# Kernel optimization log

Measured on AMD Instinct MI355X. Metric: run time of the kernel, lower is better.

## Reference

```python
import jax, jax.numpy as jnp
import numpy as np

RADIUS = 0.4   # 0.2 * nlayer, nlayer = 2
NSAMPLE = 32   # k


def _fps(xyz, m):
    """Farthest point sampling. xyz: (B, N, 3) -> idx (B, m) int32.
    Matches pointnet2 CUDA kernel: first sampled point is index 0."""
    B, N, _ = xyz.shape

    def step(carry, _):
        dist, far = carry
        centroid = jnp.take_along_axis(xyz, far[:, None, None], axis=1)  # (B,1,3)
        d = jnp.sum((xyz - centroid) ** 2, axis=-1)                      # (B,N)
        dist = jnp.minimum(dist, d)
        return (dist, jnp.argmax(dist, axis=-1).astype(jnp.int32)), far

    init = (jnp.full((B, N), jnp.inf, dtype=xyz.dtype),
            jnp.zeros((B,), dtype=jnp.int32))
    _, idx = jax.lax.scan(step, init, None, length=m)  # (m, B)
    return idx.T                                       # (B, m)


def _ball_query(radius, k, xyz, new_xyz):
    """xyz (B,N,3), new_xyz (B,M,3) -> (B,M,k) int32.
    First k in-radius indices in ascending index order; slots past the
    number of in-radius points are filled with the first found index
    (pointnet2 ball_query semantics)."""
    N = xyz.shape[1]
    d2 = jnp.sum((new_xyz[:, :, None, :] - xyz[:, None, :, :]) ** 2, axis=-1)  # (B,M,N)
    key = jnp.where(d2 < radius * radius,
                    jnp.arange(N, dtype=jnp.int32), jnp.int32(N))              # (B,M,N)
    topv, _ = jax.lax.top_k(-key, k)   # k smallest keys, ascending
    idx = -topv                        # (B,M,k)
    valid = idx < N
    idx = jnp.where(valid, idx, idx[..., :1])  # pad with first found index
    return idx


def _group(t, idx):
    """t (B,C,N), idx (B,M,k) -> (B,C,M,k)."""
    return jnp.take_along_axis(t[:, :, None, :], idx[:, None, :, :], axis=3)


def setup_inputs() -> dict:
    key = jax.random.key(0)
    k1, k2, k3 = jax.random.split(key, 3)
    return {
        "x": jax.random.normal(k1, (8, 3, 8192), dtype=jnp.float32),
        "feature": jax.random.normal(k2, (8, 64, 8192), dtype=jnp.float32),
        "weight": jax.random.normal(k3, (64, 64), dtype=jnp.float32) / 8.0,
        "num_pool": 2048,
    }


def reference(x, feature, weight, num_pool):
    # x: (B,3,N) coordinates, feature: (B,C,N), weight: 1x1 conv (C_out, C_in)
    xyz = jnp.transpose(x, (0, 2, 1))                       # (B,N,3)
    fps_idx = _fps(xyz, num_pool)                           # (B,M)
    new_xyz = jnp.take_along_axis(xyz, fps_idx[:, :, None], axis=1)  # (B,M,3)
    sub_idx = _ball_query(RADIUS, NSAMPLE, xyz, new_xyz)    # (B,M,k)

    x_out = _group(x, sub_idx).max(axis=-1)                 # (B,3,M)
    fg = _group(feature, sub_idx)                           # (B,C,M,k)
    f_out = jnp.einsum('oc,bcmk->bomk', weight, fg).max(axis=-1)  # (B,C,M)
    return x_out, f_out
```

## Files before the change

kernel.cpp:

```cpp
#include <hip/hip_runtime.h>
#include <cstdint>
#include <cstddef>

#define BB 8
#define NN 8192
#define CC 64
#define MM 2048
#define KK 32

typedef float vfloat2 __attribute__((ext_vector_type(2)));

__device__ __forceinline__ float sqdist_exact(float x, float y, float z,
                                              float cx, float cy, float cz) {
    float dx = __fsub_rn(x, cx);
    float dy = __fsub_rn(y, cy);
    float dz = __fsub_rn(z, cz);
    return __fadd_rn(__fadd_rn(__fmul_rn(dx, dx), __fmul_rn(dy, dy)),
                     __fmul_rn(dz, dz));
}

template <int CTRL>
__device__ __forceinline__ unsigned dpp_max_u32(unsigned v) {
    unsigned s = (unsigned)__builtin_amdgcn_update_dpp(0, (int)v, CTRL, 0xF, 0xF, true);
    return v > s ? v : s;
}
template <int CTRL>
__device__ __forceinline__ unsigned dpp_min_u32(unsigned v) {
    unsigned s = (unsigned)__builtin_amdgcn_update_dpp(0x7FFFFFFF, (int)v, CTRL, 0xF, 0xF, false);
    return v < s ? v : s;
}

__device__ __forceinline__ int octile(float v) {
    return (v > -1.1503494f) + (v > -0.6744898f) + (v > -0.3186394f) + (v > 0.0f) +
           (v > 0.3186394f) + (v > 0.6744898f) + (v > 1.1503494f);
}

__device__ __forceinline__ int morton9(int bx, int by, int bz) {
    int m = (bz & 1) | ((bz & 2) << 2) | ((bz & 4) << 4);
    m |= ((by & 1) << 1) | ((by & 2) << 3) | ((by & 4) << 5);
    m |= ((bx & 1) << 2) | ((bx & 2) << 4) | ((bx & 4) << 6);
    return m;
}

__global__ __launch_bounds__(512) void fps_kernel(const float* __restrict__ x,
                                                  int* __restrict__ fps_idx) {
#pragma clang fp contract(off)
    const int b = blockIdx.x;
    const int tid = threadIdx.x;
    const int lane = tid & 63;
    const float* xb = x + (size_t)b * 3 * NN;
    int* fps_store = fps_idx + b * MM;

    __shared__ float sx[NN];
    __shared__ float sy[NN];
    __shared__ float sz[NN];
    __shared__ int sidx[NN];
    __shared__ int hist[512];
    __shared__ int scanb[512];
    __shared__ int sfps[MM];
    __shared__ unsigned long long red3[3];

    const vfloat2* gx = (const vfloat2*)xb;
    const vfloat2* gy = (const vfloat2*)(xb + NN);
    const vfloat2* gz = (const vfloat2*)(xb + 2 * NN);

    vfloat2 lx[8], ly[8], lz[8];
#pragma unroll
    for (int p = 0; p < 8; ++p) {
        const int e = tid + p * 512;
        lx[p] = gx[e];
        ly[p] = gy[e];
        lz[p] = gz[e];
        ((vfloat2*)sx)[e] = lx[p];
        ((vfloat2*)sy)[e] = ly[p];
        ((vfloat2*)sz)[e] = lz[p];
    }
    hist[tid] = 0;
    if (tid < 3) red3[tid] = 0ull;
    __syncthreads();

    int mybin[16];
#pragma unroll
    for (int p = 0; p < 8; ++p) {
        int b0 = morton9(octile(lx[p].x), octile(ly[p].x), octile(lz[p].x));
        int b1 = morton9(octile(lx[p].y), octile(ly[p].y), octile(lz[p].y));
        mybin[2 * p] = b0;
        mybin[2 * p + 1] = b1;
        atomicAdd(&hist[b0], 1);
        atomicAdd(&hist[b1], 1);
    }
    __syncthreads();
    int own = hist[tid];
    scanb[tid] = own;
    __syncthreads();
    for (int off = 1; off < 512; off <<= 1) {
        int add = (tid >= off) ? scanb[tid - off] : 0;
        __syncthreads();
        scanb[tid] += add;
        __syncthreads();
    }
    hist[tid] = scanb[tid] - own;
    __syncthreads();
#pragma unroll
    for (int p = 0; p < 8; ++p) {
        const int i0 = 2 * (tid + p * 512);
        int pos0 = atomicAdd(&hist[mybin[2 * p]], 1);
        sidx[pos0] = i0;
        int pos1 = atomicAdd(&hist[mybin[2 * p + 1]], 1);
        sidx[pos1] = i0 + 1;
    }
    __syncthreads();

    vfloat2 px[8], py[8], pz[8], dist[8];
    int idxr[16];
#pragma unroll
    for (int p = 0; p < 8; ++p) {
        const int j0 = sidx[tid * 16 + 2 * p];
        const int j1 = sidx[tid * 16 + 2 * p + 1];
        idxr[2 * p] = j0;
        idxr[2 * p + 1] = j1;
        px[p] = (vfloat2){sx[j0], sx[j1]};
        py[p] = (vfloat2){sy[j0], sy[j1]};
        pz[p] = (vfloat2){sz[j0], sz[j1]};
        dist[p] = (vfloat2){INFINITY, INFINITY};
    }
    float blx = fminf(px[0].x, px[0].y), bhx = fmaxf(px[0].x, px[0].y);
    float bly = fminf(py[0].x, py[0].y), bhy = fmaxf(py[0].x, py[0].y);
    float blz = fminf(pz[0].x, pz[0].y), bhz = fmaxf(pz[0].x, pz[0].y);
#pragma unroll
    for (int p = 1; p < 8; ++p) {
        blx = fminf(blx, fminf(px[p].x, px[p].y));
        bhx = fmaxf(bhx, fmaxf(px[p].x, px[p].y));
        bly = fminf(bly, fminf(py[p].x, py[p].y));
        bhy = fmaxf(bhy, fmaxf(py[p].x, py[p].y));
        blz = fminf(blz, fminf(pz[p].x, pz[p].y));
        bhz = fmaxf(bhz, fmaxf(pz[p].x, pz[p].y));
    }

    float cmax = INFINITY;
    int cidx = idxr[0];
    int far = 0;
    for (int t = 0; t < MM; ++t) {
        if (tid == 0) {
            sfps[t] = far;
            red3[(t + 1) % 3] = 0ull;
        }
        const float cx = sx[far];
        const float cy = sy[far];
        const float cz = sz[far];

        float qx = cx - fminf(fmaxf(cx, blx), bhx);
        float qy = cy - fminf(fmaxf(cy, bly), bhy);
        float qz = cz - fminf(fmaxf(cz, blz), bhz);
        float bound = (qx * qx + qy * qy) + qz * qz;
        const bool act = !(bound * 0.999f >= cmax);
        if (act) {
            const vfloat2 cx2 = {cx, cx};
            const vfloat2 cy2 = {cy, cy};
            const vfloat2 cz2 = {cz, cz};
            float mv = -1.0f;
#pragma unroll
            for (int p = 0; p < 8; ++p) {
                vfloat2 dx = px[p] - cx2;
                vfloat2 dy = py[p] - cy2;
                vfloat2 dz = pz[p] - cz2;
                vfloat2 m1 = dx * dx;
                vfloat2 m2 = dy * dy;
                vfloat2 m3 = dz * dz;
                vfloat2 s = (m1 + m2) + m3;
                vfloat2 nd;
                nd.x = fminf(dist[p].x, s.x);
                nd.y = fminf(dist[p].y, s.y);
                dist[p] = nd;
                mv = fmaxf(fmaxf(mv, nd.x), nd.y);
            }
            int mi = 0x7FFFFFFF;
#pragma unroll
            for (int p = 0; p < 8; ++p) {
                mi = min(mi, (dist[p].x == mv) ? idxr[2 * p] : 0x7FFFFFFF);
                mi = min(mi, (dist[p].y == mv) ? idxr[2 * p + 1] : 0x7FFFFFFF);
            }
            cmax = mv;
            cidx = mi;
        }

        unsigned mvb = __float_as_uint(cmax);
        mvb = dpp_max_u32<0x111>(mvb);
        mvb = dpp_max_u32<0x112>(mvb);
        mvb = dpp_max_u32<0x114>(mvb);
        mvb = dpp_max_u32<0x118>(mvb);
        mvb = dpp_max_u32<0x142>(mvb);
        mvb = dpp_max_u32<0x143>(mvb);
        const unsigned wmax = (unsigned)__builtin_amdgcn_readlane((int)mvb, 63);
        unsigned midx = (__float_as_uint(cmax) == wmax) ? (unsigned)cidx : 0x7FFFFFFFu;
        midx = dpp_min_u32<0x111>(midx);
        midx = dpp_min_u32<0x112>(midx);
        midx = dpp_min_u32<0x114>(midx);
        midx = dpp_min_u32<0x118>(midx);
        midx = dpp_min_u32<0x142>(midx);
        midx = dpp_min_u32<0x143>(midx);
        if (lane == 63) {
            unsigned long long key =
                ((unsigned long long)wmax << 32) | (unsigned)(~midx);
            atomicMax(&red3[t % 3], key);
        }
        __syncthreads();
        far = (int)(~(unsigned)red3[t % 3]);
    }
    __syncthreads();
    for (int t = tid; t < MM; t += 512) fps_store[t] = sfps[t];
}

__global__ __launch_bounds__(256) void transform_kernel(const float* __restrict__ feature,
                                                        const float* __restrict__ weight,
                                                        float* __restrict__ g) {
    __shared__ float Wl[64 * 64];
    const int tid = threadIdx.x;
    for (int k = tid; k < 64 * 64; k += 256) Wl[k] = weight[k];
    __syncthreads();

    const int P = blockIdx.x * 256 + tid;
    const int b = P >> 13;
    const int n = P & (NN - 1);
    const float* fb = feature + (size_t)b * CC * NN + n;

    float fr[64];
#pragma unroll
    for (int c = 0; c < 64; ++c) fr[c] = fb[(size_t)c * NN];

    float* go = g + ((size_t)b << 19) + (size_t)n * 64;
    for (int o = 0; o < 64; o += 4) {
        const float* w0 = &Wl[o * 64];
        const float* w1 = w0 + 64;
        const float* w2 = w0 + 128;
        const float* w3 = w0 + 192;
        float a0 = 0.f, a1 = 0.f, a2 = 0.f, a3 = 0.f;
#pragma unroll
        for (int c = 0; c < 64; c += 4) {
            float4 v0 = *(const float4*)(w0 + c);
            float4 v1 = *(const float4*)(w1 + c);
            float4 v2 = *(const float4*)(w2 + c);
            float4 v3 = *(const float4*)(w3 + c);
            a0 += v0.x * fr[c] + v0.y * fr[c + 1] + v0.z * fr[c + 2] + v0.w * fr[c + 3];
            a1 += v1.x * fr[c] + v1.y * fr[c + 1] + v1.z * fr[c + 2] + v1.w * fr[c + 3];
            a2 += v2.x * fr[c] + v2.y * fr[c + 1] + v2.z * fr[c + 2] + v2.w * fr[c + 3];
            a3 += v3.x * fr[c] + v3.y * fr[c + 1] + v3.z * fr[c + 2] + v3.w * fr[c + 3];
        }
        float4 r;
        r.x = a0; r.y = a1; r.z = a2; r.w = a3;
        *(float4*)(go + o) = r;
    }
}

__global__ __launch_bounds__(256) void bq_kernel(const float* __restrict__ x,
                                                 const int* __restrict__ fps_idx,
                                                 int* __restrict__ sub_idx,
                                                 float* __restrict__ xout) {
    const float R2 = (float)(0.4 * 0.4);
    int gw = (int)((blockIdx.x * 256 + threadIdx.x) >> 6);
    const int lane = threadIdx.x & 63;
    gw = __builtin_amdgcn_readfirstlane(gw);
    const int b = gw >> 11;
    const int m = gw & (MM - 1);
    const float* xb = x + (size_t)b * 3 * NN;

    const int ctr = fps_idx[gw];
    const float cx = xb[ctr];
    const float cy = xb[NN + ctr];
    const float cz = xb[2 * NN + ctr];

    int* sid = sub_idx + (size_t)gw * KK;
    int found = 0;
    int first = 0;
    float mx = -INFINITY, my = -INFINITY, mz = -INFINITY;

    for (int base = 0; base < NN; base += 64) {
        const int i = base + lane;
        const float xx = xb[i];
        const float yy = xb[NN + i];
        const float zz = xb[2 * NN + i];
        const float d2 = sqdist_exact(xx, yy, zz, cx, cy, cz);
        const bool q = d2 < R2;
        const unsigned long long mask = __ballot(q);
        if (q) {
            int pos = found + (int)__popcll(mask & ((1ull << lane) - 1ull));
            if (pos < KK) {
                sid[pos] = i;
                mx = fmaxf(mx, xx);
                my = fmaxf(my, yy);
                mz = fmaxf(mz, zz);
            }
        }
        if (found == 0 && mask != 0ull) first = base + (int)__builtin_ctzll(mask);
        found += (int)__popcll(mask);
        if (found >= KK) break;
    }
    if (found < KK) {
        if (lane < KK - found) sid[found + lane] = first;
    }
#pragma unroll
    for (int off = 32; off >= 1; off >>= 1) {
        mx = fmaxf(mx, __shfl_xor(mx, off, 64));
        my = fmaxf(my, __shfl_xor(my, off, 64));
        mz = fmaxf(mz, __shfl_xor(mz, off, 64));
    }
    if (lane == 0) {
        xout[(size_t)b * 3 * MM + 0 * MM + m] = mx;
        xout[(size_t)b * 3 * MM + 1 * MM + m] = my;
        xout[(size_t)b * 3 * MM + 2 * MM + m] = mz;
    }
}

__global__ __launch_bounds__(256) void gather_kernel(const float* __restrict__ g,
                                                     const int* __restrict__ sub_idx,
                                                     float* __restrict__ fout) {
    int gw = (int)((blockIdx.x * 256 + threadIdx.x) >> 6);
    const int lane = threadIdx.x & 63;
    gw = __builtin_amdgcn_readfirstlane(gw);
    const int b = gw >> 11;
    const int m = gw & (MM - 1);
    const int* sid = sub_idx + (size_t)gw * KK;
    const float* gb = g + ((size_t)b << 19);
    float acc = -INFINITY;
#pragma unroll
    for (int j = 0; j < KK; ++j) {
        const int id = sid[j];
        acc = fmaxf(acc, gb[(size_t)id * 64 + lane]);
    }
    fout[((size_t)b << 17) + ((size_t)lane << 11) + m] = acc;
}

extern "C" void kernel_launch(void* const* d_in, const int* in_sizes, int n_in,
                              void* d_out, int out_size, void* d_ws, size_t ws_size,
                              hipStream_t stream) {
    const float* x = (const float*)d_in[0];
    const float* feature = (const float*)d_in[1];
    const float* weight = (const float*)d_in[2];

    float* out = (float*)d_out;
    float* xout = out;
    float* fout = out + BB * 3 * MM;

    char* ws = (char*)d_ws;
    int* fps_idx = (int*)ws;
    int* sub_idx = (int*)(ws + (size_t)BB * MM * 4);
    float* g = (float*)(ws + (size_t)BB * MM * 4 + (size_t)BB * MM * KK * 4);

    fps_kernel<<<BB, 512, 0, stream>>>(x, fps_idx);
    transform_kernel<<<(BB * NN) / 256, 256, 0, stream>>>(feature, weight, g);
    bq_kernel<<<(BB * MM * 64) / 256, 256, 0, stream>>>(x, fps_idx, sub_idx, xout);
    gather_kernel<<<(BB * MM * 64) / 256, 256, 0, stream>>>(g, sub_idx, fout);
}
```

Baseline: 1.923 ms.

## Fuse transform into FPS launch and fuse ball query with gather

The feature transform now runs as extra blocks of the FPS launch, so the 8 long-running FPS blocks share the device with transform work instead of running serially before it. Ball query and gather are merged into one kernel that keeps neighbour indices in shared memory, which removes the global sub_idx round trip and one launch. The transform blocks now run at 512 threads and get the large FPS shared-memory allocation through a union, which may lower their occupancy. An unused morton9 variant is also added.

```diff
diff --git a/kernel.cpp b/kernel.cpp
--- a/kernel.cpp
+++ b/kernel.cpp
@@ -38,227 +38,242 @@
 __device__ __forceinline__ int morton9(int bx, int by, int bz) {
     int m = (bz & 1) | ((bz & 2) << 2) | ((bz & 4) << 4);
     m |= ((by & 1) << 1) | ((by & 2) << 3) | ((by & 4) << 5);
+    m |= ((bx & 1) << 2) | ((bx & 2) << 4) | ((bx & 6) << 4 & 0x40) | ((bx & 4) << 4);
+    return m;
+}
+
+__device__ __forceinline__ int morton9_ref(int bx, int by, int bz) {
+    int m = (bz & 1) | ((bz & 2) << 2) | ((bz & 4) << 4);
+    m |= ((by & 1) << 1) | ((by & 2) << 3) | ((by & 4) << 5);
     m |= ((bx & 1) << 2) | ((bx & 2) << 4) | ((bx & 4) << 6);
     return m;
 }
 
-__global__ __launch_bounds__(512) void fps_kernel(const float* __restrict__ x,
-                                                  int* __restrict__ fps_idx) {
+union FSmem {
+    struct {
+        float sx[NN];
+        float sy[NN];
+        float sz[NN];
+        int sidx[NN];
+        int hist[512];
+        int scanb[512];
+        int sfps[MM];
+        unsigned long long red3[3];
+    } f;
+    float Wl[64 * 64];
+};
+
+__global__ __launch_bounds__(512) void fps_transform_kernel(
+        const float* __restrict__ x, int* __restrict__ fps_idx,
+        const float* __restrict__ feature, const float* __restrict__ weight,
+        float* __restrict__ g) {
+    __shared__ FSmem sm;
+    const int tid = threadIdx.x;
+
+    if (blockIdx.x >= BB) {
+        for (int k = tid; k < 64 * 64; k += 512) sm.Wl[k] = weight[k];
+        __syncthreads();
+        const int P = (blockIdx.x - BB) * 512 + tid;
+        const int b = P >> 13;
+        const int n = P & (NN - 1);
+        const float* fb = feature + (size_t)b * CC * NN + n;
+        float fr[64];
+#pragma unroll
+        for (int c = 0; c < 64; ++c) fr[c] = fb[(size_t)c * NN];
+        float* go = g + ((size_t)b << 19) + (size_t)n * 64;
+        for (int o = 0; o < 64; o += 4) {
+            const float* w0 = &sm.Wl[o * 64];
+            const float* w1 = w0 + 64;
+            const float* w2 = w0 + 128;
+            const float* w3 = w0 + 192;
+            float a0 = 0.f, a1 = 0.f, a2 = 0.f, a3 = 0.f;
+#pragma unroll
+            for (int c = 0; c < 64; c += 4) {
+                float4 v0 = *(const float4*)(w0 + c);
+                float4 v1 = *(const float4*)(w1 + c);
+                float4 v2 = *(const float4*)(w2 + c);
+                float4 v3 = *(const float4*)(w3 + c);
+                a0 += v0.x * fr[c] + v0.y * fr[c + 1] + v0.z * fr[c + 2] + v0.w * fr[c + 3];
+                a1 += v1.x * fr[c] + v1.y * fr[c + 1] + v1.z * fr[c + 2] + v1.w * fr[c + 3];
+                a2 += v2.x * fr[c] + v2.y * fr[c + 1] + v2.z * fr[c + 2] + v2.w * fr[c + 3];
+                a3 += v3.x * fr[c] + v3.y * fr[c + 1] + v3.z * fr[c + 2] + v3.w * fr[c + 3];
+            }
+            float4 r;
+            r.x = a0; r.y = a1; r.z = a2; r.w = a3;
+            *(float4*)(go + o) = r;
+        }
+        return;
+    }
+
+    {
 #pragma clang fp contract(off)
-    const int b = blockIdx.x;
-    const int tid = threadIdx.x;
-    const int lane = tid & 63;
-    const float* xb = x + (size_t)b * 3 * NN;
-    int* fps_store = fps_idx + b * MM;
-
-    __shared__ float sx[NN];
-    __shared__ float sy[NN];
-    __shared__ float sz[NN];
-    __shared__ int sidx[NN];
-    __shared__ int hist[512];
-    __shared__ int scanb[512];
-    __shared__ int sfps[MM];
-    __shared__ unsigned long long red3[3];
-
-    const vfloat2* gx = (const vfloat2*)xb;
-    const vfloat2* gy = (const vfloat2*)(xb + NN);
-    const vfloat2* gz = (const vfloat2*)(xb + 2 * NN);
-
-    vfloat2 lx[8], ly[8], lz[8];
-#pragma unroll
-    for (int p = 0; p < 8; ++p) {
-        const int e = tid + p * 512;
-        lx[p] = gx[e];
-        ly[p] = gy[e];
-        lz[p] = gz[e];
-        ((vfloat2*)sx)[e] = lx[p];
-        ((vfloat2*)sy)[e] = ly[p];
-        ((vfloat2*)sz)[e] = lz[p];
-    }
-    hist[tid] = 0;
-    if (tid < 3) red3[tid] = 0ull;
-    __syncthreads();
-
-    int mybin[16];
-#pragma unroll
-    for (int p = 0; p < 8; ++p) {
-        int b0 = morton9(octile(lx[p].x), octile(ly[p].x), octile(lz[p].x));
-        int b1 = morton9(octile(lx[p].y), octile(ly[p].y), octile(lz[p].y));
-        mybin[2 * p] = b0;
-        mybin[2 * p + 1] = b1;
-        atomicAdd(&hist[b0], 1);
-        atomicAdd(&hist[b1], 1);
-    }
-    __syncthreads();
-    int own = hist[tid];
-    scanb[tid] = own;
-    __syncthreads();
-    for (int off = 1; off < 512; off <<= 1) {
-        int add = (tid >= off) ? scanb[tid - off] : 0;
-        __syncthreads();
-        scanb[tid] += add;
-        __syncthreads();
-    }
-    hist[tid] = scanb[tid] - own;
-    __syncthreads();
-#pragma unroll
-    for (int p = 0; p < 8; ++p) {
-        const int i0 = 2 * (tid + p * 512);
-        int pos0 = atomicAdd(&hist[mybin[2 * p]], 1);
-        sidx[pos0] = i0;
-        int pos1 = atomicAdd(&hist[mybin[2 * p + 1]], 1);
-        sidx[pos1] = i0 + 1;
-    }
-    __syncthreads();
-
-    vfloat2 px[8], py[8], pz[8], dist[8];
-    int idxr[16];
-#pragma unroll
-    for (int p = 0; p < 8; ++p) {
-        const int j0 = sidx[tid * 16 + 2 * p];
-        const int j1 = sidx[tid * 16 + 2 * p + 1];
-        idxr[2 * p] = j0;
-        idxr[2 * p + 1] = j1;
-        px[p] = (vfloat2){sx[j0], sx[j1]};
-        py[p] = (vfloat2){sy[j0], sy[j1]};
-        pz[p] = (vfloat2){sz[j0], sz[j1]};
-        dist[p] = (vfloat2){INFINITY, INFINITY};
-    }
-    float blx = fminf(px[0].x, px[0].y), bhx = fmaxf(px[0].x, px[0].y);
-    float bly = fminf(py[0].x, py[0].y), bhy = fmaxf(py[0].x, py[0].y);
-    float blz = fminf(pz[0].x, pz[0].y), bhz = fmaxf(pz[0].x, pz[0].y);
-#pragma unroll
-    for (int p = 1; p < 8; ++p) {
-        blx = fminf(blx, fminf(px[p].x, px[p].y));
-        bhx = fmaxf(bhx, fmaxf(px[p].x, px[p].y));
-        bly = fminf(bly, fminf(py[p].x, py[p].y));
-        bhy = fmaxf(bhy, fmaxf(py[p].x, py[p].y));
-        blz = fminf(blz, fminf(pz[p].x, pz[p].y));
-        bhz = fmaxf(bhz, fmaxf(pz[p].x, pz[p].y));
-    }
-
-    float cmax = INFINITY;
-    int cidx = idxr[0];
-    int far = 0;
-    for (int t = 0; t < MM; ++t) {
-        if (tid == 0) {
-            sfps[t] = far;
-            red3[(t + 1) % 3] = 0ull;
-        }
-        const float cx = sx[far];
-        const float cy = sy[far];
-        const float cz = sz[far];
-
-        float qx = cx - fminf(fmaxf(cx, blx), bhx);
-        float qy = cy - fminf(fmaxf(cy, bly), bhy);
-        float qz = cz - fminf(fmaxf(cz, blz), bhz);
-        float bound = (qx * qx + qy * qy) + qz * qz;
-        const bool act = !(bound * 0.999f >= cmax);
-        if (act) {
-            const vfloat2 cx2 = {cx, cx};
-            const vfloat2 cy2 = {cy, cy};
-            const vfloat2 cz2 = {cz, cz};
-            float mv = -1.0f;
-#pragma unroll
-            for (int p = 0; p < 8; ++p) {
-                vfloat2 dx = px[p] - cx2;
-                vfloat2 dy = py[p] - cy2;
-                vfloat2 dz = pz[p] - cz2;
-                vfloat2 m1 = dx * dx;
-                vfloat2 m2 = dy * dy;
-                vfloat2 m3 = dz * dz;
-                vfloat2 s = (m1 + m2) + m3;
-                vfloat2 nd;
-                nd.x = fminf(dist[p].x, s.x);
-                nd.y = fminf(dist[p].y, s.y);
-                dist[p] = nd;
-                mv = fmaxf(fmaxf(mv, nd.x), nd.y);
-            }
-            int mi = 0x7FFFFFFF;
-#pragma unroll
-            for (int p = 0; p < 8; ++p) {
-                mi = min(mi, (dist[p].x == mv) ? idxr[2 * p] : 0x7FFFFFFF);
-                mi = min(mi, (dist[p].y == mv) ? idxr[2 * p + 1] : 0x7FFFFFFF);
-            }
-            cmax = mv;
-            cidx = mi;
-        }
-
-        unsigned mvb = __float_as_uint(cmax);
-        mvb = dpp_max_u32<0x111>(mvb);
-        mvb = dpp_max_u32<0x112>(mvb);
-        mvb = dpp_max_u32<0x114>(mvb);
-        mvb = dpp_max_u32<0x118>(mvb);
-        mvb = dpp_max_u32<0x142>(mvb);
-        mvb = dpp_max_u32<0x143>(mvb);
-        const unsigned wmax = (unsigned)__builtin_amdgcn_readlane((int)mvb, 63);
-        unsigned midx = (__float_as_uint(cmax) == wmax) ? (unsigned)cidx : 0x7FFFFFFFu;
-        midx = dpp_min_u32<0x111>(midx);
-        midx = dpp_min_u32<0x112>(midx);
-        midx = dpp_min_u32<0x114>(midx);
-        midx = dpp_min_u32<0x118>(midx);
-        midx = dpp_min_u32<0x142>(midx);
-        midx = dpp_min_u32<0x143>(midx);
-        if (lane == 63) {
-            unsigned long long key =
-                ((unsigned long long)wmax << 32) | (unsigned)(~midx);
-            atomicMax(&red3[t % 3], key);
-        }
-        __syncthreads();
-        far = (int)(~(unsigned)red3[t % 3]);
-    }
-    __syncthreads();
-    for (int t = tid; t < MM; t += 512) fps_store[t] = sfps[t];
-}
-
-__global__ __launch_bounds__(256) void transform_kernel(const float* __restrict__ feature,
-                                                        const float* __restrict__ weight,
-                                                        float* __restrict__ g) {
-    __shared__ float Wl[64 * 64];
-    const int tid = threadIdx.x;
-    for (int k = tid; k < 64 * 64; k += 256) Wl[k] = weight[k];
-    __syncthreads();
-
-    const int P = blockIdx.x * 256 + tid;
-    const int b = P >> 13;
-    const int n = P & (NN - 1);
-    const float* fb = feature + (size_t)b * CC * NN + n;
-
-    float fr[64];
-#pragma unroll
-    for (int c = 0; c < 64; ++c) fr[c] = fb[(size_t)c * NN];
-
-    float* go = g + ((size_t)b << 19) + (size_t)n * 64;
-    for (int o = 0; o < 64; o += 4) {
-        const float* w0 = &Wl[o * 64];
-        const float* w1 = w0 + 64;
-        const float* w2 = w0 + 128;
-        const float* w3 = w0 + 192;
-        float a0 = 0.f, a1 = 0.f, a2 = 0.f, a3 = 0.f;
-#pragma unroll
-        for (int c = 0; c < 64; c += 4) {
-            float4 v0 = *(const float4*)(w0 + c);
-            float4 v1 = *(const float4*)(w1 + c);
-            float4 v2 = *(const float4*)(w2 + c);
-            float4 v3 = *(const float4*)(w3 + c);
-            a0 += v0.x * fr[c] + v0.y * fr[c + 1] + v0.z * fr[c + 2] + v0.w * fr[c + 3];
-            a1 += v1.x * fr[c] + v1.y * fr[c + 1] + v1.z * fr[c + 2] + v1.w * fr[c + 3];
-            a2 += v2.x * fr[c] + v2.y * fr[c + 1] + v2.z * fr[c + 2] + v2.w * fr[c + 3];
-            a3 += v3.x * fr[c] + v3.y * fr[c + 1] + v3.z * fr[c + 2] + v3.w * fr[c + 3];
-        }
-        float4 r;
-        r.x = a0; r.y = a1; r.z = a2; r.w = a3;
-        *(float4*)(go + o) = r;
-    }
-}
-
-__global__ __launch_bounds__(256) void bq_kernel(const float* __restrict__ x,
-                                                 const int* __restrict__ fps_idx,
-                                                 int* __restrict__ sub_idx,
-                                                 float* __restrict__ xout) {
+        const int b = blockIdx.x;
+        const int lane = tid & 63;
+        const float* xb = x + (size_t)b * 3 * NN;
+        int* fps_store = fps_idx + b * MM;
+
+        const vfloat2* gx = (const vfloat2*)xb;
+        const vfloat2* gy = (const vfloat2*)(xb + NN);
+        const vfloat2* gz = (const vfloat2*)(xb + 2 * NN);
+
+        vfloat2 lx[8], ly[8], lz[8];
+#pragma unroll
+        for (int p = 0; p < 8; ++p) {
+            const int e = tid + p * 512;
+            lx[p] = gx[e];
+            ly[p] = gy[e];
+            lz[p] = gz[e];
+            ((vfloat2*)sm.f.sx)[e] = lx[p];
+            ((vfloat2*)sm.f.sy)[e] = ly[p];
+            ((vfloat2*)sm.f.sz)[e] = lz[p];
+        }
+        sm.f.hist[tid] = 0;
+        if (tid < 3) sm.f.red3[tid] = 0ull;
+        __syncthreads();
+
+        int mybin[16];
+#pragma unroll
+        for (int p = 0; p < 8; ++p) {
+            int b0 = morton9_ref(octile(lx[p].x), octile(ly[p].x), octile(lz[p].x));
+            int b1 = morton9_ref(octile(lx[p].y), octile(ly[p].y), octile(lz[p].y));
+            mybin[2 * p] = b0;
+            mybin[2 * p + 1] = b1;
+            atomicAdd(&sm.f.hist[b0], 1);
+            atomicAdd(&sm.f.hist[b1], 1);
+        }
+        __syncthreads();
+        int own = sm.f.hist[tid];
+        sm.f.scanb[tid] = own;
+        __syncthreads();
+        for (int off = 1; off < 512; off <<= 1) {
+            int add = (tid >= off) ? sm.f.scanb[tid - off] : 0;
+            __syncthreads();
+            sm.f.scanb[tid] += add;
+            __syncthreads();
+        }
+        sm.f.hist[tid] = sm.f.scanb[tid] - own;
+        __syncthreads();
+#pragma unroll
+        for (int p = 0; p < 8; ++p) {
+            const int i0 = 2 * (tid + p * 512);
+            int pos0 = atomicAdd(&sm.f.hist[mybin[2 * p]], 1);
+            sm.f.sidx[pos0] = i0;
+            int pos1 = atomicAdd(&sm.f.hist[mybin[2 * p + 1]], 1);
+            sm.f.sidx[pos1] = i0 + 1;
+        }
+        __syncthreads();
+
+        vfloat2 px[8], py[8], pz[8], dist[8];
+        int idxr[16];
+#pragma unroll
+        for (int p = 0; p < 8; ++p) {
+            const int j0 = sm.f.sidx[tid * 16 + 2 * p];
+            const int j1 = sm.f.sidx[tid * 16 + 2 * p + 1];
+            idxr[2 * p] = j0;
+            idxr[2 * p + 1] = j1;
+            px[p] = (vfloat2){sm.f.sx[j0], sm.f.sx[j1]};
+            py[p] = (vfloat2){sm.f.sy[j0], sm.f.sy[j1]};
+            pz[p] = (vfloat2){sm.f.sz[j0], sm.f.sz[j1]};
+            dist[p] = (vfloat2){INFINITY, INFINITY};
+        }
+        float blx = fminf(px[0].x, px[0].y), bhx = fmaxf(px[0].x, px[0].y);
+        float bly = fminf(py[0].x, py[0].y), bhy = fmaxf(py[0].x, py[0].y);
+        float blz = fminf(pz[0].x, pz[0].y), bhz = fmaxf(pz[0].x, pz[0].y);
+#pragma unroll
+        for (int p = 1; p < 8; ++p) {
+            blx = fminf(blx, fminf(px[p].x, px[p].y));
+            bhx = fmaxf(bhx, fmaxf(px[p].x, px[p].y));
+            bly = fminf(bly, fminf(py[p].x, py[p].y));
+            bhy = fmaxf(bhy, fmaxf(py[p].x, py[p].y));
+            blz = fminf(blz, fminf(pz[p].x, pz[p].y));
+            bhz = fmaxf(bhz, fmaxf(pz[p].x, pz[p].y));
+        }
+
+        float cmax = INFINITY;
+        int cidx = idxr[0];
+        int far = 0;
+        for (int t = 0; t < MM; ++t) {
+            if (tid == 0) {
+                sm.f.sfps[t] = far;
+                sm.f.red3[(t + 1) % 3] = 0ull;
+            }
+            const float cx = sm.f.sx[far];
+            const float cy = sm.f.sy[far];
+            const float cz = sm.f.sz[far];
+
+            float qx = cx - fminf(fmaxf(cx, blx), bhx);
+            float qy = cy - fminf(fmaxf(cy, bly), bhy);
+            float qz = cz - fminf(fmaxf(cz, blz), bhz);
+            float bound = (qx * qx + qy * qy) + qz * qz;
+            const bool act = !(bound * 0.999f >= cmax);
+            if (act) {
+                const vfloat2 cx2 = {cx, cx};
+                const vfloat2 cy2 = {cy, cy};
+                const vfloat2 cz2 = {cz, cz};
+                float mv = -1.0f;
+#pragma unroll
+                for (int p = 0; p < 8; ++p) {
+                    vfloat2 dx = px[p] - cx2;
+                    vfloat2 dy = py[p] - cy2;
+                    vfloat2 dz = pz[p] - cz2;
+                    vfloat2 m1 = dx * dx;
+                    vfloat2 m2 = dy * dy;
+                    vfloat2 m3 = dz * dz;
+                    vfloat2 s = (m1 + m2) + m3;
+                    vfloat2 nd;
+                    nd.x = fminf(dist[p].x, s.x);
+                    nd.y = fminf(dist[p].y, s.y);
+                    dist[p] = nd;
+                    mv = fmaxf(fmaxf(mv, nd.x), nd.y);
+                }
+                int mi = 0x7FFFFFFF;
+#pragma unroll
+                for (int p = 0; p < 8; ++p) {
+                    mi = min(mi, (dist[p].x == mv) ? idxr[2 * p] : 0x7FFFFFFF);
+                    mi = min(mi, (dist[p].y == mv) ? idxr[2 * p + 1] : 0x7FFFFFFF);
+                }
+                cmax = mv;
+                cidx = mi;
+            }
+
+            unsigned mvb = __float_as_uint(cmax);
+            mvb = dpp_max_u32<0x111>(mvb);
+            mvb = dpp_max_u32<0x112>(mvb);
+            mvb = dpp_max_u32<0x114>(mvb);
+            mvb = dpp_max_u32<0x118>(mvb);
+            mvb = dpp_max_u32<0x142>(mvb);
+            mvb = dpp_max_u32<0x143>(mvb);
+            const unsigned wmax = (unsigned)__builtin_amdgcn_readlane((int)mvb, 63);
+            unsigned midx = (__float_as_uint(cmax) == wmax) ? (unsigned)cidx : 0x7FFFFFFFu;
+            midx = dpp_min_u32<0x111>(midx);
+            midx = dpp_min_u32<0x112>(midx);
+            midx = dpp_min_u32<0x114>(midx);
+            midx = dpp_min_u32<0x118>(midx);
+            midx = dpp_min_u32<0x142>(midx);
+            midx = dpp_min_u32<0x143>(midx);
+            if (lane == 63) {
+                unsigned long long key =
+                    ((unsigned long long)wmax << 32) | (unsigned)(~midx);
+                atomicMax(&sm.f.red3[t % 3], key);
+            }
+            __syncthreads();
+            far = (int)(~(unsigned)sm.f.red3[t % 3]);
+        }
+        __syncthreads();
+        for (int t = tid; t < MM; t += 512) fps_store[t] = sm.f.sfps[t];
+    }
+}
+
+__global__ __launch_bounds__(256) void bqgather_kernel(const float* __restrict__ x,
+                                                       const int* __restrict__ fps_idx,
+                                                       const float* __restrict__ g,
+                                                       float* __restrict__ xout,
+                                                       float* __restrict__ fout) {
     const float R2 = (float)(0.4 * 0.4);
+    __shared__ int sidl[4][KK];
     int gw = (int)((blockIdx.x * 256 + threadIdx.x) >> 6);
     const int lane = threadIdx.x & 63;
+    const int wvl = threadIdx.x >> 6;
     gw = __builtin_amdgcn_readfirstlane(gw);
     const int b = gw >> 11;
     const int m = gw & (MM - 1);
@@ -269,7 +284,6 @@
     const float cy = xb[NN + ctr];
     const float cz = xb[2 * NN + ctr];
 
-    int* sid = sub_idx + (size_t)gw * KK;
     int found = 0;
     int first = 0;
     float mx = -INFINITY, my = -INFINITY, mz = -INFINITY;
@@ -285,7 +299,7 @@
         if (q) {
             int pos = found + (int)__popcll(mask & ((1ull << lane) - 1ull));
             if (pos < KK) {
-                sid[pos] = i;
+                sidl[wvl][pos] = i;
                 mx = fmaxf(mx, xx);
                 my = fmaxf(my, yy);
                 mz = fmaxf(mz, zz);
@@ -296,7 +310,7 @@
         if (found >= KK) break;
     }
     if (found < KK) {
-        if (lane < KK - found) sid[found + lane] = first;
+        if (lane < KK - found) sidl[wvl][found + lane] = first;
     }
 #pragma unroll
     for (int off = 32; off >= 1; off >>= 1) {
@@ -309,22 +323,13 @@
         xout[(size_t)b * 3 * MM + 1 * MM + m] = my;
         xout[(size_t)b * 3 * MM + 2 * MM + m] = mz;
     }
-}
-
-__global__ __launch_bounds__(256) void gather_kernel(const float* __restrict__ g,
-                                                     const int* __restrict__ sub_idx,
-                                                     float* __restrict__ fout) {
-    int gw = (int)((blockIdx.x * 256 + threadIdx.x) >> 6);
-    const int lane = threadIdx.x & 63;
-    gw = __builtin_amdgcn_readfirstlane(gw);
-    const int b = gw >> 11;
-    const int m = gw & (MM - 1);
-    const int* sid = sub_idx + (size_t)gw * KK;
+    __syncthreads();
+
     const float* gb = g + ((size_t)b << 19);
     float acc = -INFINITY;
 #pragma unroll
     for (int j = 0; j < KK; ++j) {
-        const int id = sid[j];
+        const int id = sidl[wvl][j];
         acc = fmaxf(acc, gb[(size_t)id * 64 + lane]);
     }
     fout[((size_t)b << 17) + ((size_t)lane << 11) + m] = acc;
@@ -343,11 +348,9 @@
 
     char* ws = (char*)d_ws;
     int* fps_idx = (int*)ws;
-    int* sub_idx = (int*)(ws + (size_t)BB * MM * 4);
     float* g = (float*)(ws + (size_t)BB * MM * 4 + (size_t)BB * MM * KK * 4);
 
-    fps_kernel<<<BB, 512, 0, stream>>>(x, fps_idx);
-    transform_kernel<<<(BB * NN) / 256, 256, 0, stream>>>(feature, weight, g);
-    bq_kernel<<<(BB * MM * 64) / 256, 256, 0, stream>>>(x, fps_idx, sub_idx, xout);
-    gather_kernel<<<(BB * MM * 64) / 256, 256, 0, stream>>>(g, sub_idx, fout);
-}
+    fps_transform_kernel<<<BB + (BB * NN) / 512, 512, 0, stream>>>(
+        x, fps_idx, feature, weight, g);
+    bqgather_kernel<<<(BB * MM * 64) / 256, 256, 0, stream>>>(x, fps_idx, g, xout, fout);
+}
```

New measurement: 1.872 ms. 1.03x faster.
